# Kernel optimization log

Hardware: AMD Instinct MI355X
Metric: run time of the kernel (lower is better)

## Reference

```python
import jax, jax.numpy as jnp
import numpy as np

N, T, D = 32, 64, 16
F = 512  # object_classes == feature dim after object_fc


def _gcn(x, adj, W, b):
    # Kipf GraphConvolution: adj @ (x @ W) + b
    return adj @ (x @ W) + b


def _norm_adj(a):
    d = jnp.sum(a, axis=1) ** -0.5
    return a * d[:, None] * d[None, :]


def _per_graph(x, gc1_W, gc1_b, gc2_W, gc2_b, gc3_W, gc3_b, gc4_W, gc4_b):
    # x: [D, F]
    # graph_generator / adj2: softmax-style similarity adjacency with D^{-1/2} norm
    s = x @ x.T                                   # [D, D]
    a = jnp.exp(s - jnp.max(s, axis=1, keepdims=True))
    adj = _norm_adj(a)
    # branch 1
    x1 = jax.nn.relu(_gcn(x, adj, gc1_W, gc1_b))
    x1 = _gcn(x1, adj, gc2_W, gc2_b)
    # branch 2 (adj_hat2 identical construction from x)
    y2 = jax.nn.relu(_gcn(x, adj, gc3_W, gc3_b))  # [D, 32]
    y22 = y2 @ y2.T
    nrm = jnp.sqrt(jnp.sum(y22 * y22, axis=1, keepdims=True))  # torch.norm(y22, 2, dim=1)
    adj3 = 1.0 + y22 / (nrm @ nrm.T)
    adj_hat3 = _norm_adj(adj3)
    y2 = _gcn(y2, adj_hat3, gc4_W, gc4_b)
    return (x1 + y2) * 0.5


def setup_inputs() -> dict:
    key = jax.random.key(0)
    ks = jax.random.split(key, 12)
    s = 0.02
    return {
        "object_raw": jax.random.normal(ks[0], (N * T * D, F), jnp.float32),
        "action_raw": jax.random.normal(ks[1], (N * T, F), jnp.float32),
        "W_obj": jax.random.normal(ks[2], (F, 512), jnp.float32) * s,
        "b_obj": jnp.zeros((512,), jnp.float32),
        "W_act": jax.random.normal(ks[3], (F, 512), jnp.float32) * s,
        "b_act": jnp.zeros((512,), jnp.float32),
        "gc1_W": jax.random.normal(ks[4], (512, 32), jnp.float32) * s,
        "gc1_b": jnp.zeros((32,), jnp.float32),
        "gc2_W": jax.random.normal(ks[5], (32, 512), jnp.float32) * s,
        "gc2_b": jnp.zeros((512,), jnp.float32),
        "gc3_W": jax.random.normal(ks[6], (512, 32), jnp.float32) * s,
        "gc3_b": jnp.zeros((32,), jnp.float32),
        "gc4_W": jax.random.normal(ks[7], (32, 512), jnp.float32) * s,
        "gc4_b": jnp.zeros((512,), jnp.float32),
        "fc1_W": jax.random.normal(ks[8], (512, 1024), jnp.float32) * s,
        "fc1_b": jnp.zeros((1024,), jnp.float32),
        "clf_W": jax.random.normal(ks[9], (1024, 500), jnp.float32) * s,
        "clf_b": jnp.zeros((500,), jnp.float32),
    }


def reference(object_raw, action_raw, W_obj, b_obj, W_act, b_act,
              gc1_W, gc1_b, gc2_W, gc2_b, gc3_W, gc3_b, gc4_W, gc4_b,
              fc1_W, fc1_b, clf_W, clf_b):
    obj = jax.nn.relu(object_raw @ W_obj + b_obj).reshape(N * T, D, 512)
    act = jax.nn.relu(action_raw @ W_act + b_act)           # [N*T, 512]
    obj = obj.at[:, D // 2].set(act)                         # overwrite middle frame
    graph = jax.vmap(lambda x: _per_graph(x, gc1_W, gc1_b, gc2_W, gc2_b,
                                          gc3_W, gc3_b, gc4_W, gc4_b))(obj)
    g = graph.reshape(N, T, D, 512).mean(axis=2)
    o = obj.reshape(N, T, D, 512).mean(axis=2)
    feat = (o + g) * 0.5                                     # graph_fusion == 'mean'
    c = jax.nn.relu(feat)                                    # dropout = identity (eval)
    c = jax.nn.relu(c @ fc1_W + fc1_b)
    out = (c @ clf_W + clf_b).mean(axis=1)                   # mean over T -> [N, 500]
    return out
```

## Files before the change

kernel.cpp:

```cpp
#include <hip/hip_runtime.h>
#include <hip/hip_bf16.h>

using ushort_t = unsigned short;
using f32x4  = __attribute__((ext_vector_type(4))) float;
using short8 = __attribute__((ext_vector_type(8))) short;

__device__ __forceinline__ float bflo(unsigned p) {
    union { unsigned u; float f; } x; x.u = p << 16; return x.f;
}
__device__ __forceinline__ float bfhi(unsigned p) {
    union { unsigned u; float f; } x; x.u = p & 0xffff0000u; return x.f;
}
__device__ __forceinline__ ushort_t f2bf(float f) {
    __hip_bfloat16 h = __float2bfloat16(f);
    return *(ushort_t*)&h;
}
__device__ __forceinline__ unsigned pk2bf(float lo, float hi) {
    __hip_bfloat162 h = __float22bfloat162_rn({lo, hi});
    return *(unsigned*)&h;
}

__device__ __forceinline__ void tr_tile(const float* __restrict__ S, ushort_t* __restrict__ D,
                                        int K, int N, int Npad, int bx, int by,
                                        int tx, int ty, float* tile )
{
    const int k0 = by * 32, n0 = bx * 32;
#pragma unroll
    for (int r = 0; r < 4; r++) {
        const int k = k0 + ty + r * 8, n = n0 + tx;
        tile[(ty + r * 8) * 33 + tx] = (k < K && n < N) ? S[(size_t)k * N + n] : 0.f;
    }
    __syncthreads();
#pragma unroll
    for (int r = 0; r < 4; r++) {
        const int n = n0 + ty + r * 8, k = k0 + tx;
        if (n < Npad && k < K) D[(size_t)n * K + k] = f2bf(tile[tx * 33 + ty + r * 8]);
    }
}

__device__ __forceinline__ void trf_tile(const float* __restrict__ S, float* __restrict__ D,
                                         int K, int N, int bx, int by,
                                         int tx, int ty, float* tile )
{
    const int k0 = by * 32, n0 = bx * 32;
#pragma unroll
    for (int r = 0; r < 4; r++) {
        const int k = k0 + ty + r * 8, n = n0 + tx;
        tile[(ty + r * 8) * 33 + tx] = (k < K && n < N) ? S[(size_t)k * N + n] : 0.f;
    }
    __syncthreads();
#pragma unroll
    for (int r = 0; r < 4; r++) {
        const int n = n0 + ty + r * 8, k = k0 + tx;
        if (n < N && k < K) D[(size_t)n * K + k] = tile[tx * 33 + ty + r * 8];
    }
}

__global__ __launch_bounds__(256)
void prep_weights(const float* __restrict__ Wobj, ushort_t* __restrict__ WobjT,
                  const float* __restrict__ Wact, ushort_t* __restrict__ WactT,
                  const float* __restrict__ fc1W, ushort_t* __restrict__ fc1T,
                  const float* __restrict__ gc1W, ushort_t* __restrict__ W1t,
                  const float* __restrict__ gc3W, ushort_t* __restrict__ W3t,
                  const float* __restrict__ gc2W, ushort_t* __restrict__ W2bf,
                  const float* __restrict__ gc4W, ushort_t* __restrict__ W4bf,
                  const float* __restrict__ clfW, float* __restrict__ WclfT)
{
    __shared__ float tile[32 * 33];
    const int b = blockIdx.x;
    const int t = threadIdx.x;
    const int tx = t & 31, ty = t >> 5;

    if (b < 1056) {
        const float* S; ushort_t* D; int K, N, Npad, nt, l;
        if      (b < 256)  { S = Wobj; D = WobjT; K = 512; N = 512;  Npad = 512;  nt = 16; l = b; }
        else if (b < 512)  { S = Wact; D = WactT; K = 512; N = 512;  Npad = 512;  nt = 16; l = b - 256; }
        else if (b < 1024) { S = fc1W; D = fc1T;  K = 512; N = 1024; Npad = 1024; nt = 32; l = b - 512; }
        else if (b < 1040) { S = gc1W; D = W1t;   K = 512; N = 32;   Npad = 32;   nt = 1;  l = b - 1024; }
        else               { S = gc3W; D = W3t;   K = 512; N = 32;   Npad = 32;   nt = 1;  l = b - 1040; }
        tr_tile(S, D, K, N, Npad, l % nt, l / nt, tx, ty, tile);
    } else if (b < 1072) {
        const float* S = (b < 1064) ? gc2W : gc4W;
        ushort_t* D    = (b < 1064) ? W2bf : W4bf;
        const int i = (b < 1064 ? b - 1056 : b - 1064) * 256 + t;
        const float4 x = ((const float4*)S)[2 * i];
        const float4 y = ((const float4*)S)[2 * i + 1];
        unsigned r[4] = { pk2bf(x.x, x.y), pk2bf(x.z, x.w), pk2bf(y.x, y.y), pk2bf(y.z, y.w) };
        ((uint4*)D)[i] = *(uint4*)r;
    } else {
        const int l = b - 1072;
        trf_tile(clfW, WclfT, 1024, 500, l & 15, l >> 4, tx, ty, tile);
    }
}

typedef __attribute__((address_space(1))) void glb_void;
typedef __attribute__((address_space(3))) void lds_void;
__device__ __forceinline__ void dma16(const void* g, void* l) {
    __builtin_amdgcn_global_load_lds((glb_void*)(unsigned long long)(uintptr_t)g,
                                     (lds_void*)(unsigned)(uintptr_t)l, 16, 0, 0);
}

template<int RELU, typename AT>
__global__ __launch_bounds__(256)
void gemm_dma(const AT* __restrict__ A, const ushort_t* __restrict__ Bt,
              const float* __restrict__ bias, ushort_t* __restrict__ C,
              int N, int K, int Nb, int row_mul, int row_add)
{
    __shared__ __align__(16) char     AsRaw[128 * 32 * sizeof(AT)];
    __shared__ __align__(16) ushort_t Bs[128 * 32];
    const int t = threadIdx.x;
    const int lane = t & 63, w = t >> 6;
    const int bm = blockIdx.y * 128, bn = blockIdx.x * 128;
    const int mb = (w & 1) * 64, nb = (w >> 1) * 64;
    const int fr = lane & 15, fq = lane >> 4;

    f32x4 acc[16];
#pragma unroll
    for (int i = 0; i < 16; i++) acc[i] = (f32x4){0.f, 0.f, 0.f, 0.f};

    const int brow = lane >> 2, bk = lane & 3;
    const int klog = bk ^ ((brow >> 1) & 3);
    const int arow = lane >> 3, ag = lane & 7;

    for (int k0 = 0; k0 < K; k0 += 32) {
        __syncthreads();
        if constexpr (sizeof(AT) == 4) {
#pragma unroll
            for (int i = 0; i < 4; i++) {
                const int grp = w * 4 + i;
                const int row = grp * 8 + arow;
                const int gl = ag ^ (row & 7);
                dma16((const float*)A + (size_t)(bm + row) * K + k0 + gl * 4,
                      AsRaw + grp * 1024);
            }
        } else {
#pragma unroll
            for (int i = 0; i < 2; i++) {
                const int grp = w * 2 + i;
                const int row = grp * 16 + brow;
                dma16((const ushort_t*)A + (size_t)(bm + row) * K + k0 + klog * 8,
                      (ushort_t*)AsRaw + grp * 512);
            }
        }
#pragma unroll
        for (int i = 0; i < 2; i++) {
            const int grp = w * 2 + i;
            const int row = grp * 16 + brow;
            dma16(Bt + (size_t)(bn + row) * K + k0 + klog * 8, Bs + grp * 512);
        }
        __syncthreads();

        short8 af[4], bf[4];
        if constexpr (sizeof(AT) == 4) {
#pragma unroll
            for (int i = 0; i < 4; i++) {
                const int row = mb + i * 16 + fr;
                const float* base = (const float*)AsRaw + row * 32;
                const f32x4 p0 = *(const f32x4*)(base + (((2 * fq)     ^ (fr & 7)) * 4));
                const f32x4 p1 = *(const f32x4*)(base + (((2 * fq + 1) ^ (fr & 7)) * 4));
                unsigned rr[4] = { pk2bf(p0.x, p0.y), pk2bf(p0.z, p0.w),
                                   pk2bf(p1.x, p1.y), pk2bf(p1.z, p1.w) };
                af[i] = *(short8*)rr;
            }
        } else {
#pragma unroll
            for (int i = 0; i < 4; i++) {
                const int row = mb + i * 16 + fr;
                af[i] = *(const short8*)((const ushort_t*)AsRaw + row * 32 + (fq ^ ((fr >> 1) & 3)) * 8);
            }
        }
#pragma unroll
        for (int j = 0; j < 4; j++) {
            const int row = nb + j * 16 + fr;
            bf[j] = *(const short8*)(Bs + row * 32 + (fq ^ ((fr >> 1) & 3)) * 8);
        }
#pragma unroll
        for (int i = 0; i < 4; i++)
#pragma unroll
            for (int j = 0; j < 4; j++)
                acc[i * 4 + j] = __builtin_amdgcn_mfma_f32_16x16x32_bf16(
                    af[i], bf[j], acc[i * 4 + j], 0, 0, 0);
    }

#pragma unroll
    for (int j = 0; j < 4; j++) {
        const int n = bn + nb + j * 16 + fr;
        const float bv = (n < Nb) ? bias[n] : 0.f;
#pragma unroll
        for (int i = 0; i < 4; i++) {
            const f32x4 a = acc[i * 4 + j];
#pragma unroll
            for (int r = 0; r < 4; r++) {
                const int m = bm + mb + i * 16 + fq * 4 + r;
                float v = a[r] + bv;
                if (RELU) v = fmaxf(v, 0.f);
                C[((size_t)m * row_mul + row_add) * (size_t)N + n] = f2bf(v);
            }
        }
    }
}

__global__ __launch_bounds__(256)
void gemm_fc1_mean(const ushort_t* __restrict__ A, const ushort_t* __restrict__ Bt,
                   const float* __restrict__ bias, float* __restrict__ cmean)
{
    __shared__ __align__(16) ushort_t AsS[128 * 32];
    __shared__ __align__(16) ushort_t Bs[128 * 32];
    const int t = threadIdx.x;
    const int lane = t & 63, w = t >> 6;
    const int bm = blockIdx.y * 128, bn = blockIdx.x * 128;
    const int mb = (w & 1) * 64, nb = (w >> 1) * 64;
    const int fr = lane & 15, fq = lane >> 4;
    const int K = 512;

    f32x4 acc[16];
#pragma unroll
    for (int i = 0; i < 16; i++) acc[i] = (f32x4){0.f, 0.f, 0.f, 0.f};

    const int brow = lane >> 2, bk = lane & 3;
    const int klog = bk ^ ((brow >> 1) & 3);

    for (int k0 = 0; k0 < K; k0 += 32) {
        __syncthreads();
#pragma unroll
        for (int i = 0; i < 2; i++) {
            const int grp = w * 2 + i;
            const int row = grp * 16 + brow;
            dma16(A + (size_t)(bm + row) * K + k0 + klog * 8, AsS + grp * 512);
        }
#pragma unroll
        for (int i = 0; i < 2; i++) {
            const int grp = w * 2 + i;
            const int row = grp * 16 + brow;
            dma16(Bt + (size_t)(bn + row) * K + k0 + klog * 8, Bs + grp * 512);
        }
        __syncthreads();

        short8 af[4], bf[4];
#pragma unroll
        for (int i = 0; i < 4; i++) {
            const int row = mb + i * 16 + fr;
            af[i] = *(const short8*)(AsS + row * 32 + (fq ^ ((fr >> 1) & 3)) * 8);
        }
#pragma unroll
        for (int j = 0; j < 4; j++) {
            const int row = nb + j * 16 + fr;
            bf[j] = *(const short8*)(Bs + row * 32 + (fq ^ ((fr >> 1) & 3)) * 8);
        }
#pragma unroll
        for (int i = 0; i < 4; i++)
#pragma unroll
            for (int j = 0; j < 4; j++)
                acc[i * 4 + j] = __builtin_amdgcn_mfma_f32_16x16x32_bf16(
                    af[i], bf[j], acc[i * 4 + j], 0, 0, 0);
    }

    const int nidx = (bm + mb) >> 6;
#pragma unroll
    for (int j = 0; j < 4; j++) {
        const int n = bn + nb + j * 16 + fr;
        const float bv = bias[n];
        float s = 0.f;
#pragma unroll
        for (int i = 0; i < 4; i++) {
            const f32x4 a = acc[i * 4 + j];
#pragma unroll
            for (int r = 0; r < 4; r++) s += fmaxf(a[r] + bv, 0.f);
        }
        s += __shfl_xor(s, 16);
        s += __shfl_xor(s, 32);
        if (fq == 0) cmean[(size_t)nidx * 1024 + n] = s * (1.0f / 64.0f);
    }
}

__global__ __launch_bounds__(1024, 4)
void mega_obj_graph(const float* __restrict__ A, const ushort_t* __restrict__ Bt,
                    const float* __restrict__ bias, const ushort_t* __restrict__ act_bf,
                    const ushort_t* __restrict__ W1t, const ushort_t* __restrict__ W3t,
                    const float* __restrict__ b1, const float* __restrict__ b3,
                    const ushort_t* __restrict__ W2b, const float* __restrict__ b2,
                    const ushort_t* __restrict__ W4b, const float* __restrict__ b4,
                    ushort_t* __restrict__ cbuf)
{
    __shared__ __align__(16) ushort_t As[128 * 512];
    __shared__ __align__(16) float fsS[8][992];

    const int t = threadIdx.x;
    const int lane = t & 63, w = t >> 6;
    const int bm = blockIdx.x * 128;
    const int fr = lane & 15, fq = lane >> 4;

    const float4* A4 = (const float4*)(A + (size_t)bm * 512);
#pragma unroll
    for (int i = 0; i < 8; i++) {
        const int fl = i * 2048 + t * 2;
        const int row = fl >> 7;
        const float4 p0 = A4[fl];
        const float4 p1 = A4[fl + 1];
        unsigned rr[4] = { pk2bf(p0.x, p0.y), pk2bf(p0.z, p0.w),
                           pk2bf(p1.x, p1.y), pk2bf(p1.z, p1.w) };
        *(uint4*)&As[row * 512 + ((lane ^ (row & 7)) * 8)] = *(uint4*)rr;
    }

    const int nw = w * 32;
    const ushort_t* Bbase = Bt + (size_t)(nw + fr) * 512 + fq * 8;
    uint4 bA[2], bB[2];
#pragma unroll
    for (int j = 0; j < 2; j++) bA[j] = *(const uint4*)(Bbase + (size_t)j * 16 * 512);

    __syncthreads();

    f32x4 acc[2][8];
#pragma unroll
    for (int j = 0; j < 2; j++)
#pragma unroll
        for (int i = 0; i < 8; i++) acc[j][i] = (f32x4){0.f, 0.f, 0.f, 0.f};

    for (int kk = 0; kk < 16; kk += 2) {
        short8 af[8];
#pragma unroll
        for (int i = 0; i < 8; i++)
            af[i] = *(const short8*)&As[(i * 16 + fr) * 512 + (((kk * 4 + fq) ^ (fr & 7)) * 8)];
#pragma unroll
        for (int j = 0; j < 2; j++) {
            bB[j] = *(const uint4*)(Bbase + (size_t)j * 16 * 512 + (kk + 1) * 32);
            const short8 bf = *(const short8*)&bA[j];
#pragma unroll
            for (int i = 0; i < 8; i++)
                acc[j][i] = __builtin_amdgcn_mfma_f32_16x16x32_bf16(af[i], bf, acc[j][i], 0, 0, 0);
        }
#pragma unroll
        for (int i = 0; i < 8; i++)
            af[i] = *(const short8*)&As[(i * 16 + fr) * 512 + ((((kk + 1) * 4 + fq) ^ (fr & 7)) * 8)];
#pragma unroll
        for (int j = 0; j < 2; j++) {
            if (kk + 2 < 16)
                bA[j] = *(const uint4*)(Bbase + (size_t)j * 16 * 512 + (kk + 2) * 32);
            const short8 bf = *(const short8*)&bB[j];
#pragma unroll
            for (int i = 0; i < 8; i++)
                acc[j][i] = __builtin_amdgcn_mfma_f32_16x16x32_bf16(af[i], bf, acc[j][i], 0, 0, 0);
        }
    }

    __syncthreads();
#pragma unroll
    for (int j = 0; j < 2; j++) {
        const int col0 = nw + j * 16 + fr;
        const float bv = bias[col0];
#pragma unroll
        for (int i = 0; i < 8; i++) {
#pragma unroll
            for (int rr2 = 0; rr2 < 4; rr2++) {
                const int m = i * 16 + fq * 4 + rr2;
                As[m * 512 + ((((col0 >> 3) ^ (m & 7)) << 3) | (col0 & 7))]
                    = f2bf(fmaxf(acc[j][i][rr2] + bv, 0.f));
            }
        }
    }
    __syncthreads();

    if (t < 512) {
        const int ra = t >> 6, gg = t & 63;
        const uint4 v = *(const uint4*)(act_bf + (size_t)(blockIdx.x * 8 + ra) * 512 + gg * 8);
        *(uint4*)&As[(ra * 16 + 8) * 512 + gg * 8] = v;
    }
    __syncthreads();

    f32x4 ea = (f32x4){0.f,0.f,0.f,0.f}, eb = ea, ec = ea, ed = ea;
    float om[8] = {0,0,0,0,0,0,0,0};
    if (w < 8) {
        for (int kk = 0; kk < 16; kk++) {
            const short8 xf = *(const short8*)&As[(w * 16 + fr) * 512 + (((kk * 4 + fq) ^ (fr & 7)) * 8)];
            const short8 w10 = *(const short8*)(W1t + (size_t)fr * 512 + kk * 32 + fq * 8);
            const short8 w11 = *(const short8*)(W1t + (size_t)(16 + fr) * 512 + kk * 32 + fq * 8);
            const short8 w30 = *(const short8*)(W3t + (size_t)fr * 512 + kk * 32 + fq * 8);
            const short8 w31 = *(const short8*)(W3t + (size_t)(16 + fr) * 512 + kk * 32 + fq * 8);
            ea = __builtin_amdgcn_mfma_f32_16x16x32_bf16(xf, w10, ea, 0, 0, 0);
            eb = __builtin_amdgcn_mfma_f32_16x16x32_bf16(xf, w11, eb, 0, 0, 0);
            ec = __builtin_amdgcn_mfma_f32_16x16x32_bf16(xf, w30, ec, 0, 0, 0);
            ed = __builtin_amdgcn_mfma_f32_16x16x32_bf16(xf, w31, ed, 0, 0, 0);
        }
    } else {
        const int g = w - 8;
        for (int kk = 0; kk < 16; kk++) {
            const short8 xf = *(const short8*)&As[(g * 16 + fr) * 512 + (((kk * 4 + fq) ^ (fr & 7)) * 8)];
            ea = __builtin_amdgcn_mfma_f32_16x16x32_bf16(xf, xf, ea, 0, 0, 0);
        }
#pragma unroll
        for (int m = 0; m < 16; m++) {
            const uint4 q = *(const uint4*)&As[(g * 16 + m) * 512 + ((lane ^ (m & 7)) * 8)];
            om[0] += bflo(q.x); om[1] += bfhi(q.x);
            om[2] += bflo(q.y); om[3] += bfhi(q.y);
            om[4] += bflo(q.z); om[5] += bfhi(q.z);
            om[6] += bflo(q.w); om[7] += bfhi(q.w);
        }
    }
    __syncthreads();

    float* Hs = (float*)As;
    if (w < 8) {
        float* dst = Hs + w * 1792;
#pragma unroll
        for (int i = 0; i < 4; i++) {
            const int m = fq * 4 + i;
            dst[256 + m * 32 + fr]      = ea[i];
            dst[256 + m * 32 + 16 + fr] = eb[i];
            dst[768 + m * 32 + fr]      = ec[i];
            dst[768 + m * 32 + 16 + fr] = ed[i];
        }
    } else {
        const int g = w - 8;
        float* dst = Hs + g * 1792;
#pragma unroll
        for (int i = 0; i < 4; i++) {
            const int m = fq * 4 + i;
            dst[m * 16 + fr] = ea[i];
        }
        *(float4*)(dst + 1280 + lane * 8)     = (float4){om[0], om[1], om[2], om[3]};
        *(float4*)(dst + 1280 + lane * 8 + 4) = (float4){om[4], om[5], om[6], om[7]};
    }
    __syncthreads();

    const int r = fr, q = fq;
    const float* Hg = Hs + (w & 7) * 1792;
    float* fw   = fsS[w & 7];
    float* adjS = fw;
    float* y2S  = fw + 272;
    float* dvS  = fw + 848;
    float* cAS  = fw + 864;
    float* nrmS = fw + 880;
    float* dv3S = fw + 896;
    float* cA3S = fw + 912;
    float* zc1S = fw + 928;
    float* zc4S = fw + 960;

    float e0s = 0.f, e1s = 0.f, e2s = 0.f, e3s = 0.f, dv = 0.f;
    if (w < 8) {
        const float4 sv = *(const float4*)(Hg + r * 16 + q * 4);
        float mx = fmaxf(fmaxf(sv.x, sv.y), fmaxf(sv.z, sv.w));
        mx = fmaxf(mx, __shfl_xor(mx, 16));
        mx = fmaxf(mx, __shfl_xor(mx, 32));
        e0s = expf(sv.x - mx); e1s = expf(sv.y - mx);
        e2s = expf(sv.z - mx); e3s = expf(sv.w - mx);
        float rs = e0s + e1s + e2s + e3s;
        rs += __shfl_xor(rs, 16); rs += __shfl_xor(rs, 32);
        dv = rsqrtf(rs);
        if (q == 0) dvS[r] = dv;
    }
    __syncthreads();

    if (w < 8) {
        const float4 dc = *(const float4*)&dvS[q * 4];
        const float ad0 = e0s * dv * dc.x, ad1 = e1s * dv * dc.y;
        const float ad2 = e2s * dv * dc.z, ad3 = e3s * dv * dc.w;
        adjS[r * 17 + q * 4 + 0] = ad0; adjS[r * 17 + q * 4 + 1] = ad1;
        adjS[r * 17 + q * 4 + 2] = ad2; adjS[r * 17 + q * 4 + 3] = ad3;
        float c0s = ad0, c1s = ad1, c2s = ad2, c3s = ad3;
#pragma unroll
        for (int m = 1; m <= 8; m <<= 1) {
            c0s += __shfl_xor(c0s, m); c1s += __shfl_xor(c1s, m);
            c2s += __shfl_xor(c2s, m); c3s += __shfl_xor(c3s, m);
        }
        if (r == 0) {
            cAS[q * 4 + 0] = c0s; cAS[q * 4 + 1] = c1s;
            cAS[q * 4 + 2] = c2s; cAS[q * 4 + 3] = c3s;
        }
    }
    __syncthreads();

    const int c0 = q * 8;
    float x1v[8], y2v[8];
    if (w < 8) {
        const float4 b1a = *(const float4*)(b1 + c0);
        const float4 b1b = *(const float4*)(b1 + c0 + 4);
        const float4 b3a = *(const float4*)(b3 + c0);
        const float4 b3b = *(const float4*)(b3 + c0 + 4);
        x1v[0]=b1a.x; x1v[1]=b1a.y; x1v[2]=b1a.z; x1v[3]=b1a.w;
        x1v[4]=b1b.x; x1v[5]=b1b.y; x1v[6]=b1b.z; x1v[7]=b1b.w;
        y2v[0]=b3a.x; y2v[1]=b3a.y; y2v[2]=b3a.z; y2v[3]=b3a.w;
        y2v[4]=b3b.x; y2v[5]=b3b.y; y2v[6]=b3b.z; y2v[7]=b3b.w;
#pragma unroll
        for (int j = 0; j < 16; j++) {
            const float a = adjS[r * 17 + j];
            const float4 t1a = *(const float4*)(Hg + 256 + j * 32 + c0);
            const float4 t1b = *(const float4*)(Hg + 256 + j * 32 + c0 + 4);
            const float4 t3a = *(const float4*)(Hg + 768 + j * 32 + c0);
            const float4 t3b = *(const float4*)(Hg + 768 + j * 32 + c0 + 4);
            x1v[0] = fmaf(a, t1a.x, x1v[0]); x1v[1] = fmaf(a, t1a.y, x1v[1]);
            x1v[2] = fmaf(a, t1a.z, x1v[2]); x1v[3] = fmaf(a, t1a.w, x1v[3]);
            x1v[4] = fmaf(a, t1b.x, x1v[4]); x1v[5] = fmaf(a, t1b.y, x1v[5]);
            x1v[6] = fmaf(a, t1b.z, x1v[6]); x1v[7] = fmaf(a, t1b.w, x1v[7]);
            y2v[0] = fmaf(a, t3a.x, y2v[0]); y2v[1] = fmaf(a, t3a.y, y2v[1]);
            y2v[2] = fmaf(a, t3a.z, y2v[2]); y2v[3] = fmaf(a, t3a.w, y2v[3]);
            y2v[4] = fmaf(a, t3b.x, y2v[4]); y2v[5] = fmaf(a, t3b.y, y2v[5]);
            y2v[6] = fmaf(a, t3b.z, y2v[6]); y2v[7] = fmaf(a, t3b.w, y2v[7]);
        }
#pragma unroll
        for (int cc = 0; cc < 8; cc++) {
            x1v[cc] = fmaxf(x1v[cc], 0.f);
            y2v[cc] = fmaxf(y2v[cc], 0.f);
            y2S[r * 36 + c0 + cc] = y2v[cc];
        }
    }
    __syncthreads();

    float yy[4] = {0.f, 0.f, 0.f, 0.f};
    if (w < 8) {
#pragma unroll
        for (int k4 = 0; k4 < 8; k4++) {
            const float4 yi = *(const float4*)&y2S[r * 36 + k4 * 4];
#pragma unroll
            for (int i = 0; i < 4; i++) {
                const float4 yj = *(const float4*)&y2S[(q * 4 + i) * 36 + k4 * 4];
                yy[i] = fmaf(yi.x, yj.x, yy[i]); yy[i] = fmaf(yi.y, yj.y, yy[i]);
                yy[i] = fmaf(yi.z, yj.z, yy[i]); yy[i] = fmaf(yi.w, yj.w, yy[i]);
            }
        }
        float sq = 0.f;
#pragma unroll
        for (int i = 0; i < 4; i++) sq = fmaf(yy[i], yy[i], sq);
        sq += __shfl_xor(sq, 16); sq += __shfl_xor(sq, 32);
        const float nr = sqrtf(sq);
        if (q == 0) nrmS[r] = nr;
    }
    __syncthreads();

    float a3[4] = {0.f, 0.f, 0.f, 0.f};
    float dv3 = 0.f;
    if (w < 8) {
        const float nr = nrmS[r];
        const float4 ncv = *(const float4*)&nrmS[q * 4];
        a3[0] = 1.0f + yy[0] / (nr * ncv.x);
        a3[1] = 1.0f + yy[1] / (nr * ncv.y);
        a3[2] = 1.0f + yy[2] / (nr * ncv.z);
        a3[3] = 1.0f + yy[3] / (nr * ncv.w);
        float d3 = a3[0] + a3[1] + a3[2] + a3[3];
        d3 += __shfl_xor(d3, 16); d3 += __shfl_xor(d3, 32);
        dv3 = rsqrtf(d3);
        if (q == 0) dv3S[r] = dv3;
        const float cAm = cAS[r];
        float zp[8];
#pragma unroll
        for (int cc = 0; cc < 8; cc++) zp[cc] = cAm * x1v[cc];
#pragma unroll
        for (int m = 1; m <= 8; m <<= 1)
#pragma unroll
            for (int cc = 0; cc < 8; cc++) zp[cc] += __shfl_xor(zp[cc], m);
        if (r == 0)
#pragma unroll
            for (int cc = 0; cc < 8; cc++) zc1S[c0 + cc] = zp[cc];
    }
    __syncthreads();

    if (w < 8) {
        const float4 d3c = *(const float4*)&dv3S[q * 4];
        float p0 = a3[0] * dv3 * d3c.x, p1 = a3[1] * dv3 * d3c.y;
        float p2 = a3[2] * dv3 * d3c.z, p3 = a3[3] * dv3 * d3c.w;
#pragma unroll
        for (int m = 1; m <= 8; m <<= 1) {
            p0 += __shfl_xor(p0, m); p1 += __shfl_xor(p1, m);
            p2 += __shfl_xor(p2, m); p3 += __shfl_xor(p3, m);
        }
        if (r == 0) {
            cA3S[q * 4 + 0] = p0; cA3S[q * 4 + 1] = p1;
            cA3S[q * 4 + 2] = p2; cA3S[q * 4 + 3] = p3;
        }
    }
    __syncthreads();

    if (w < 8) {
        const float cA3m = cA3S[r];
        float zp[8];
#pragma unroll
        for (int cc = 0; cc < 8; cc++) zp[cc] = cA3m * y2v[cc];
#pragma unroll
        for (int m = 1; m <= 8; m <<= 1)
#pragma unroll
            for (int cc = 0; cc < 8; cc++) zp[cc] += __shfl_xor(zp[cc], m);
        if (r == 0)
#pragma unroll
            for (int cc = 0; cc < 8; cc++) zc4S[c0 + cc] = zp[cc];
    }
    __syncthreads();

    if (w < 8) {
        float gm[8] = {0,0,0,0,0,0,0,0};
        const ushort_t* w2p = W2b + lane * 8;
        const ushort_t* w4p = W4b + lane * 8;
#pragma unroll 8
        for (int k = 0; k < 32; k++) {
            const float z1 = zc1S[k], z4 = zc4S[k];
            const uint4 u2 = *(const uint4*)(w2p + (size_t)k * 512);
            const uint4 u4 = *(const uint4*)(w4p + (size_t)k * 512);
            gm[0] = fmaf(z1, bflo(u2.x), gm[0]); gm[0] = fmaf(z4, bflo(u4.x), gm[0]);
            gm[1] = fmaf(z1, bfhi(u2.x), gm[1]); gm[1] = fmaf(z4, bfhi(u4.x), gm[1]);
            gm[2] = fmaf(z1, bflo(u2.y), gm[2]); gm[2] = fmaf(z4, bflo(u4.y), gm[2]);
            gm[3] = fmaf(z1, bfhi(u2.y), gm[3]); gm[3] = fmaf(z4, bfhi(u4.y), gm[3]);
            gm[4] = fmaf(z1, bflo(u2.z), gm[4]); gm[4] = fmaf(z4, bflo(u4.z), gm[4]);
            gm[5] = fmaf(z1, bfhi(u2.z), gm[5]); gm[5] = fmaf(z4, bfhi(u4.z), gm[5]);
            gm[6] = fmaf(z1, bflo(u2.w), gm[6]); gm[6] = fmaf(z4, bflo(u4.w), gm[6]);
            gm[7] = fmaf(z1, bfhi(u2.w), gm[7]); gm[7] = fmaf(z4, bfhi(u4.w), gm[7]);
        }
        const float4 oma = *(const float4*)(Hg + 1280 + lane * 8);
        const float4 omb = *(const float4*)(Hg + 1280 + lane * 8 + 4);
        const float omv[8] = {oma.x, oma.y, oma.z, oma.w, omb.x, omb.y, omb.z, omb.w};
        const float4 b2a = *(const float4*)(b2 + lane * 8);
        const float4 b2b = *(const float4*)(b2 + lane * 8 + 4);
        const float4 b4a = *(const float4*)(b4 + lane * 8);
        const float4 b4b = *(const float4*)(b4 + lane * 8 + 4);
        const float bs[8] = { b2a.x + b4a.x, b2a.y + b4a.y, b2a.z + b4a.z, b2a.w + b4a.w,
                              b2b.x + b4b.x, b2b.y + b4b.y, b2b.z + b4b.z, b2b.w + b4b.w };
        ushort_t pk[8];
#pragma unroll
        for (int cc = 0; cc < 8; cc++) {
            const float gmean = 0.5f * bs[cc] + gm[cc] * (1.0f / 32.0f);
            const float feat  = 0.5f * (omv[cc] * 0.0625f + gmean);
            pk[cc] = f2bf(fmaxf(feat, 0.f));
        }
        *(uint4*)(cbuf + (size_t)(blockIdx.x * 8 + w) * 512 + lane * 8) = *(uint4*)pk;
    }
}

__global__ __launch_bounds__(256)
void clf_col(const float* __restrict__ cmean, const float* __restrict__ Wt,
             const float* __restrict__ clf_b, float* __restrict__ out)
{
    __shared__ float red[8][33];
    const int j = blockIdx.x;
    const int t = threadIdx.x;
    const int n = t & 31, kp = t >> 5;
    const float* cm = cmean + (size_t)n * 1024 + kp * 128;
    const float* wp = Wt + (size_t)j * 1024 + kp * 128;
    float acc = 0.f;
#pragma unroll
    for (int k = 0; k < 128; k += 4) {
        const float4 c = *(const float4*)(cm + k);
        const float4 wv = *(const float4*)(wp + k);
        acc = fmaf(c.x, wv.x, acc);
        acc = fmaf(c.y, wv.y, acc);
        acc = fmaf(c.z, wv.z, acc);
        acc = fmaf(c.w, wv.w, acc);
    }
    red[kp][n] = acc;
    __syncthreads();
    if (t < 32) {
        float s = red[0][t];
#pragma unroll
        for (int p = 1; p < 8; p++) s += red[p][t];
        out[(size_t)t * 500 + j] = s + clf_b[j];
    }
}

extern "C" void kernel_launch(void* const* d_in, const int* in_sizes, int n_in,
                              void* d_out, int out_size, void* d_ws, size_t ws_size,
                              hipStream_t stream)
{
    const float* object_raw = (const float*)d_in[0];
    const float* action_raw = (const float*)d_in[1];
    const float* W_obj = (const float*)d_in[2];
    const float* b_obj = (const float*)d_in[3];
    const float* W_act = (const float*)d_in[4];
    const float* b_act = (const float*)d_in[5];
    const float* gc1_W = (const float*)d_in[6];
    const float* gc1_b = (const float*)d_in[7];
    const float* gc2_W = (const float*)d_in[8];
    const float* gc2_b = (const float*)d_in[9];
    const float* gc3_W = (const float*)d_in[10];
    const float* gc3_b = (const float*)d_in[11];
    const float* gc4_W = (const float*)d_in[12];
    const float* gc4_b = (const float*)d_in[13];
    const float* fc1_W = (const float*)d_in[14];
    const float* fc1_b = (const float*)d_in[15];
    const float* clf_W = (const float*)d_in[16];
    const float* clf_b = (const float*)d_in[17];

    char* ws = (char*)d_ws;
    const size_t MB = 1024 * 1024;
    ushort_t* act_bf = (ushort_t*)(ws);
    ushort_t* cbuf   = (ushort_t*)(ws + 2 * MB);
    float*    WclfT  = (float*)   (ws + 4 * MB);
    float*    cmean  = (float*)   (ws + 6 * MB);
    ushort_t* WobjT  = (ushort_t*)(ws + 7 * MB);
    ushort_t* WactT  = (ushort_t*)(ws + 7 * MB + 512 * 1024);
    ushort_t* fc1T   = (ushort_t*)(ws + 8 * MB);
    ushort_t* W1t    = (ushort_t*)(ws + 9 * MB);
    ushort_t* W3t    = (ushort_t*)(ws + 9 * MB + 32 * 1024);
    ushort_t* W2bf   = (ushort_t*)(ws + 9 * MB + 64 * 1024);
    ushort_t* W4bf   = (ushort_t*)(ws + 9 * MB + 96 * 1024);

    prep_weights<<<dim3(1584), 256, 0, stream>>>(
        W_obj, WobjT, W_act, WactT, fc1_W, fc1T,
        gc1_W, W1t, gc3_W, W3t, gc2_W, W2bf, gc4_W, W4bf,
        clf_W, WclfT);

    gemm_dma<1, float><<<dim3(4, 16), 256, 0, stream>>>(
        action_raw, WactT, b_act, act_bf, 512, 512, 512, 1, 0);

    mega_obj_graph<<<dim3(256), 1024, 0, stream>>>(
        object_raw, WobjT, b_obj, act_bf, W1t, W3t,
        gc1_b, gc3_b, W2bf, gc2_b, W4bf, gc4_b, cbuf);

    gemm_fc1_mean<<<dim3(8, 16), 256, 0, stream>>>(cbuf, fc1T, fc1_b, cmean);

    clf_col<<<dim3(500), 256, 0, stream>>>(cmean, WclfT, clf_b, (float*)d_out);
}
```

Baseline: 222.7 us.

## Halve mega kernel block to 64 rows with 512 threads and 512 blocks

```diff
diff --git a/kernel.cpp b/kernel.cpp
--- a/kernel.cpp
+++ b/kernel.cpp
@@ -273,7 +273,7 @@
     }
 }
 
-__global__ __launch_bounds__(1024, 4)
+__global__ __launch_bounds__(512, 2)
 void mega_obj_graph(const float* __restrict__ A, const ushort_t* __restrict__ Bt,
                     const float* __restrict__ bias, const ushort_t* __restrict__ act_bf,
                     const ushort_t* __restrict__ W1t, const ushort_t* __restrict__ W3t,
@@ -282,18 +282,17 @@
                     const ushort_t* __restrict__ W4b, const float* __restrict__ b4,
                     ushort_t* __restrict__ cbuf)
 {
-    __shared__ __align__(16) ushort_t As[128 * 512];
-    __shared__ __align__(16) float fsS[8][992];
+    __shared__ __align__(16) ushort_t As[64 * 512];
 
     const int t = threadIdx.x;
     const int lane = t & 63, w = t >> 6;
-    const int bm = blockIdx.x * 128;
+    const int bm = blockIdx.x * 64;
     const int fr = lane & 15, fq = lane >> 4;
 
     const float4* A4 = (const float4*)(A + (size_t)bm * 512);
 #pragma unroll
     for (int i = 0; i < 8; i++) {
-        const int fl = i * 2048 + t * 2;
+        const int fl = i * 1024 + t * 2;
         const int row = fl >> 7;
         const float4 p0 = A4[fl];
         const float4 p1 = A4[fl + 1];
@@ -302,74 +301,74 @@
         *(uint4*)&As[row * 512 + ((lane ^ (row & 7)) * 8)] = *(uint4*)rr;
     }
 
-    const int nw = w * 32;
+    const int nw = w * 64;
     const ushort_t* Bbase = Bt + (size_t)(nw + fr) * 512 + fq * 8;
-    uint4 bA[2], bB[2];
-#pragma unroll
-    for (int j = 0; j < 2; j++) bA[j] = *(const uint4*)(Bbase + (size_t)j * 16 * 512);
-
-    __syncthreads();
-
-    f32x4 acc[2][8];
-#pragma unroll
-    for (int j = 0; j < 2; j++)
-#pragma unroll
-        for (int i = 0; i < 8; i++) acc[j][i] = (f32x4){0.f, 0.f, 0.f, 0.f};
+    uint4 bA[4], bB[4];
+#pragma unroll
+    for (int j = 0; j < 4; j++) bA[j] = *(const uint4*)(Bbase + (size_t)j * 16 * 512);
+
+    __syncthreads();
+
+    f32x4 acc[4][4];
+#pragma unroll
+    for (int i = 0; i < 4; i++)
+#pragma unroll
+        for (int j = 0; j < 4; j++) acc[i][j] = (f32x4){0.f, 0.f, 0.f, 0.f};
 
     for (int kk = 0; kk < 16; kk += 2) {
-        short8 af[8];
-#pragma unroll
-        for (int i = 0; i < 8; i++)
+        short8 af[4];
+#pragma unroll
+        for (int i = 0; i < 4; i++)
             af[i] = *(const short8*)&As[(i * 16 + fr) * 512 + (((kk * 4 + fq) ^ (fr & 7)) * 8)];
 #pragma unroll
-        for (int j = 0; j < 2; j++) {
+        for (int j = 0; j < 4; j++) {
             bB[j] = *(const uint4*)(Bbase + (size_t)j * 16 * 512 + (kk + 1) * 32);
             const short8 bf = *(const short8*)&bA[j];
 #pragma unroll
-            for (int i = 0; i < 8; i++)
-                acc[j][i] = __builtin_amdgcn_mfma_f32_16x16x32_bf16(af[i], bf, acc[j][i], 0, 0, 0);
-        }
-#pragma unroll
-        for (int i = 0; i < 8; i++)
+            for (int i = 0; i < 4; i++)
+                acc[i][j] = __builtin_amdgcn_mfma_f32_16x16x32_bf16(af[i], bf, acc[i][j], 0, 0, 0);
+        }
+#pragma unroll
+        for (int i = 0; i < 4; i++)
             af[i] = *(const short8*)&As[(i * 16 + fr) * 512 + ((((kk + 1) * 4 + fq) ^ (fr & 7)) * 8)];
 #pragma unroll
-        for (int j = 0; j < 2; j++) {
+        for (int j = 0; j < 4; j++) {
             if (kk + 2 < 16)
                 bA[j] = *(const uint4*)(Bbase + (size_t)j * 16 * 512 + (kk + 2) * 32);
             const short8 bf = *(const short8*)&bB[j];
 #pragma unroll
-            for (int i = 0; i < 8; i++)
-                acc[j][i] = __builtin_amdgcn_mfma_f32_16x16x32_bf16(af[i], bf, acc[j][i], 0, 0, 0);
-        }
-    }
-
-    __syncthreads();
-#pragma unroll
-    for (int j = 0; j < 2; j++) {
+            for (int i = 0; i < 4; i++)
+                acc[i][j] = __builtin_amdgcn_mfma_f32_16x16x32_bf16(af[i], bf, acc[i][j], 0, 0, 0);
+        }
+    }
+
+    __syncthreads();
+#pragma unroll
+    for (int j = 0; j < 4; j++) {
         const int col0 = nw + j * 16 + fr;
         const float bv = bias[col0];
 #pragma unroll
-        for (int i = 0; i < 8; i++) {
+        for (int i = 0; i < 4; i++) {
 #pragma unroll
             for (int rr2 = 0; rr2 < 4; rr2++) {
                 const int m = i * 16 + fq * 4 + rr2;
                 As[m * 512 + ((((col0 >> 3) ^ (m & 7)) << 3) | (col0 & 7))]
-                    = f2bf(fmaxf(acc[j][i][rr2] + bv, 0.f));
+                    = f2bf(fmaxf(acc[i][j][rr2] + bv, 0.f));
             }
         }
     }
     __syncthreads();
 
-    if (t < 512) {
+    if (t < 256) {
         const int ra = t >> 6, gg = t & 63;
-        const uint4 v = *(const uint4*)(act_bf + (size_t)(blockIdx.x * 8 + ra) * 512 + gg * 8);
+        const uint4 v = *(const uint4*)(act_bf + (size_t)(blockIdx.x * 4 + ra) * 512 + gg * 8);
         *(uint4*)&As[(ra * 16 + 8) * 512 + gg * 8] = v;
     }
     __syncthreads();
 
     f32x4 ea = (f32x4){0.f,0.f,0.f,0.f}, eb = ea, ec = ea, ed = ea;
     float om[8] = {0,0,0,0,0,0,0,0};
-    if (w < 8) {
+    if (w < 4) {
         for (int kk = 0; kk < 16; kk++) {
             const short8 xf = *(const short8*)&As[(w * 16 + fr) * 512 + (((kk * 4 + fq) ^ (fr & 7)) * 8)];
             const short8 w10 = *(const short8*)(W1t + (size_t)fr * 512 + kk * 32 + fq * 8);
@@ -382,7 +381,7 @@
             ed = __builtin_amdgcn_mfma_f32_16x16x32_bf16(xf, w31, ed, 0, 0, 0);
         }
     } else {
-        const int g = w - 8;
+        const int g = w - 4;
         for (int kk = 0; kk < 16; kk++) {
             const short8 xf = *(const short8*)&As[(g * 16 + fr) * 512 + (((kk * 4 + fq) ^ (fr & 7)) * 8)];
             ea = __builtin_amdgcn_mfma_f32_16x16x32_bf16(xf, xf, ea, 0, 0, 0);
@@ -399,8 +398,8 @@
     __syncthreads();
 
     float* Hs = (float*)As;
-    if (w < 8) {
-        float* dst = Hs + w * 1792;
+    if (w < 4) {
+        float* dst = Hs + (size_t)w * 4096;
 #pragma unroll
         for (int i = 0; i < 4; i++) {
             const int m = fq * 4 + i;
@@ -410,8 +409,8 @@
             dst[768 + m * 32 + 16 + fr] = ed[i];
         }
     } else {
-        const int g = w - 8;
-        float* dst = Hs + g * 1792;
+        const int g = w - 4;
+        float* dst = Hs + (size_t)g * 4096;
 #pragma unroll
         for (int i = 0; i < 4; i++) {
             const int m = fq * 4 + i;
@@ -423,20 +422,21 @@
     __syncthreads();
 
     const int r = fr, q = fq;
-    const float* Hg = Hs + (w & 7) * 1792;
-    float* fw   = fsS[w & 7];
-    float* adjS = fw;
-    float* y2S  = fw + 272;
-    float* dvS  = fw + 848;
-    float* cAS  = fw + 864;
-    float* nrmS = fw + 880;
-    float* dv3S = fw + 896;
-    float* cA3S = fw + 912;
-    float* zc1S = fw + 928;
-    float* zc4S = fw + 960;
+    float* Hg   = Hs + (size_t)(w & 3) * 4096;
+    float* x1S  = Hg + 1792;
+    float* adjS = Hg + 2304;
+    float* y2S  = Hg + 2576;
+    float* dvS  = Hg + 3152;
+    float* cAS  = Hg + 3168;
+    float* nrmS = Hg + 3184;
+    float* dv3S = Hg + 3200;
+    float* cA3S = Hg + 3216;
+    float* zc1S = Hg + 3232;
+    float* zc4S = Hg + 3264;
+    const int c0 = q * 8;
 
     float e0s = 0.f, e1s = 0.f, e2s = 0.f, e3s = 0.f, dv = 0.f;
-    if (w < 8) {
+    if (w < 4) {
         const float4 sv = *(const float4*)(Hg + r * 16 + q * 4);
         float mx = fmaxf(fmaxf(sv.x, sv.y), fmaxf(sv.z, sv.w));
         mx = fmaxf(mx, __shfl_xor(mx, 16));
@@ -450,7 +450,7 @@
     }
     __syncthreads();
 
-    if (w < 8) {
+    if (w < 4) {
         const float4 dc = *(const float4*)&dvS[q * 4];
         const float ad0 = e0s * dv * dc.x, ad1 = e1s * dv * dc.y;
         const float ad2 = e2s * dv * dc.z, ad3 = e3s * dv * dc.w;
@@ -469,9 +469,8 @@
     }
     __syncthreads();
 
-    const int c0 = q * 8;
-    float x1v[8], y2v[8];
-    if (w < 8) {
+    if (w < 4) {
+        float x1v[8], y2v[8];
         const float4 b1a = *(const float4*)(b1 + c0);
         const float4 b1b = *(const float4*)(b1 + c0 + 4);
         const float4 b3a = *(const float4*)(b3 + c0);
@@ -498,15 +497,14 @@
         }
 #pragma unroll
         for (int cc = 0; cc < 8; cc++) {
-            x1v[cc] = fmaxf(x1v[cc], 0.f);
-            y2v[cc] = fmaxf(y2v[cc], 0.f);
-            y2S[r * 36 + c0 + cc] = y2v[cc];
+            x1S[r * 32 + c0 + cc] = fmaxf(x1v[cc], 0.f);
+            y2S[r * 36 + c0 + cc] = fmaxf(y2v[cc], 0.f);
         }
     }
     __syncthreads();
 
     float yy[4] = {0.f, 0.f, 0.f, 0.f};
-    if (w < 8) {
+    if (w < 4) {
 #pragma unroll
         for (int k4 = 0; k4 < 8; k4++) {
             const float4 yi = *(const float4*)&y2S[r * 36 + k4 * 4];
@@ -528,7 +526,7 @@
 
     float a3[4] = {0.f, 0.f, 0.f, 0.f};
     float dv3 = 0.f;
-    if (w < 8) {
+    if (w < 4) {
         const float nr = nrmS[r];
         const float4 ncv = *(const float4*)&nrmS[q * 4];
         a3[0] = 1.0f + yy[0] / (nr * ncv.x);
@@ -540,9 +538,10 @@
         dv3 = rsqrtf(d3);
         if (q == 0) dv3S[r] = dv3;
         const float cAm = cAS[r];
-        float zp[8];
-#pragma unroll
-        for (int cc = 0; cc < 8; cc++) zp[cc] = cAm * x1v[cc];
+        const float4 xa = *(const float4*)&x1S[r * 32 + c0];
+        const float4 xb = *(const float4*)&x1S[r * 32 + c0 + 4];
+        float zp[8] = { cAm * xa.x, cAm * xa.y, cAm * xa.z, cAm * xa.w,
+                        cAm * xb.x, cAm * xb.y, cAm * xb.z, cAm * xb.w };
 #pragma unroll
         for (int m = 1; m <= 8; m <<= 1)
 #pragma unroll
@@ -553,7 +552,7 @@
     }
     __syncthreads();
 
-    if (w < 8) {
+    if (w < 4) {
         const float4 d3c = *(const float4*)&dv3S[q * 4];
         float p0 = a3[0] * dv3 * d3c.x, p1 = a3[1] * dv3 * d3c.y;
         float p2 = a3[2] * dv3 * d3c.z, p3 = a3[3] * dv3 * d3c.w;
@@ -569,11 +568,12 @@
     }
     __syncthreads();
 
-    if (w < 8) {
+    if (w < 4) {
         const float cA3m = cA3S[r];
-        float zp[8];
-#pragma unroll
-        for (int cc = 0; cc < 8; cc++) zp[cc] = cA3m * y2v[cc];
+        const float4 ya = *(const float4*)&y2S[r * 36 + c0];
+        const float4 yb = *(const float4*)&y2S[r * 36 + c0 + 4];
+        float zp[8] = { cA3m * ya.x, cA3m * ya.y, cA3m * ya.z, cA3m * ya.w,
+                        cA3m * yb.x, cA3m * yb.y, cA3m * yb.z, cA3m * yb.w };
 #pragma unroll
         for (int m = 1; m <= 8; m <<= 1)
 #pragma unroll
@@ -584,7 +584,7 @@
     }
     __syncthreads();
 
-    if (w < 8) {
+    if (w < 4) {
         float gm[8] = {0,0,0,0,0,0,0,0};
         const ushort_t* w2p = W2b + lane * 8;
         const ushort_t* w4p = W4b + lane * 8;
@@ -618,7 +618,7 @@
             const float feat  = 0.5f * (omv[cc] * 0.0625f + gmean);
             pk[cc] = f2bf(fmaxf(feat, 0.f));
         }
-        *(uint4*)(cbuf + (size_t)(blockIdx.x * 8 + w) * 512 + lane * 8) = *(uint4*)pk;
+        *(uint4*)(cbuf + (size_t)(blockIdx.x * 4 + w) * 512 + lane * 8) = *(uint4*)pk;
     }
 }
 
@@ -697,7 +697,7 @@
     gemm_dma<1, float><<<dim3(4, 16), 256, 0, stream>>>(
         action_raw, WactT, b_act, act_bf, 512, 512, 512, 1, 0);
 
-    mega_obj_graph<<<dim3(256), 1024, 0, stream>>>(
+    mega_obj_graph<<<dim3(512), 512, 0, stream>>>(
         object_raw, WobjT, b_obj, act_bf, W1t, W3t,
         gc1_b, gc3_b, W2bf, gc2_b, W4bf, gc4_b, cbuf);
 
```

New measurement: 233.0 us. 1.05x slower.
